# Kernel tuning notes

Measured on AMD Instinct MI355X. Metric: run time of the kernel, lower is better.

## Reference

```python
import jax, jax.numpy as jnp
import numpy as np

B, NQ, C, NH, NP = 4, 16384, 256, 8, 4
HH, WW = 128, 128
HD = C // NH


def setup_inputs() -> dict:
    key = jax.random.key(0)
    ks = jax.random.split(key, 10)
    s = 1.0 / np.sqrt(C)
    return {
        'query': jax.random.normal(ks[0], (B, NQ, C), jnp.float32),
        'reference_points': jax.random.uniform(ks[1], (B, NQ, 2), jnp.float32),
        'value': jax.random.normal(ks[2], (B, HH * WW, C), jnp.float32),
        'W_off': (jax.random.normal(ks[3], (C, NH * NP * 2), jnp.float32) * 0.01),
        'b_off': (jax.random.normal(ks[4], (NH * NP * 2,), jnp.float32) * 0.5),
        'W_attn': (jax.random.normal(ks[5], (C, NH * NP), jnp.float32) * s),
        'b_attn': jnp.zeros((NH * NP,), jnp.float32),
        'W_v': (jax.random.normal(ks[6], (C, C), jnp.float32) * s),
        'b_v': jnp.zeros((C,), jnp.float32),
        'W_out': (jax.random.normal(ks[7], (C, C), jnp.float32) * s),
        'b_out': jnp.zeros((C,), jnp.float32),
        'H': HH,
        'Wd': WW,
    }


def _deform_attn(query, reference_points, value, W_off, b_off, W_attn, b_attn,
                 W_v, b_v, W_out, b_out, H, W):
    Bb, Nq, Cc = query.shape
    dt = query.dtype
    # sampling offsets [B,Nq,NH,NP,2] and softmax attention weights [B,Nq,NH,NP]
    offsets = (query @ W_off + b_off).reshape(Bb, Nq, NH, NP, 2)
    attn = jax.nn.softmax((query @ W_attn + b_attn).reshape(Bb, Nq, NH, NP), axis=-1)
    offsets = offsets / jnp.array([W, H], dt) * jnp.asarray(0.1, dt)
    loc = jnp.clip(reference_points[:, :, None, None, :] + offsets, 0.0, 1.0)
    # value projection -> per-head spatial maps, flattened HW: [B,NH,H*W,HD]
    v = (value @ W_v + b_v).reshape(Bb, H, W, NH, HD)
    v = v.transpose(0, 3, 1, 2, 4).reshape(Bb, NH, H * W, HD)
    # grid_sample bilinear, align_corners=False, zero padding:
    # grid g = loc*2-1 ; pixel = ((g+1)*size - 1)/2 = loc*size - 0.5
    ix = loc[..., 0] * W - 0.5  # [B,Nq,NH,NP]
    iy = loc[..., 1] * H - 0.5
    x0 = jnp.floor(ix); y0 = jnp.floor(iy)
    wx = ix - x0; wy = iy - y0
    x0i = x0.astype(jnp.int32); y0i = y0.astype(jnp.int32)

    def corner(xc, yc, w):
        inb = ((xc >= 0) & (xc < W) & (yc >= 0) & (yc < H)).astype(dt)
        idx = jnp.clip(yc, 0, H - 1) * W + jnp.clip(xc, 0, W - 1)  # [B,Nq,NH,NP]
        idx = idx.transpose(0, 2, 1, 3).reshape(Bb, NH, Nq * NP)
        g = jnp.take_along_axis(v, idx[..., None], axis=2)  # [B,NH,Nq*NP,HD]
        g = g.reshape(Bb, NH, Nq, NP, HD)
        return g * (w * inb).transpose(0, 2, 1, 3)[..., None]

    one = jnp.asarray(1.0, dt)
    samp = (corner(x0i, y0i, (one - wx) * (one - wy))
            + corner(x0i + 1, y0i, wx * (one - wy))
            + corner(x0i, y0i + 1, (one - wx) * wy)
            + corner(x0i + 1, y0i + 1, wx * wy))  # [B,NH,Nq,NP,HD]
    # weighted sum over points, concat heads -> [B,Nq,C]
    out = jnp.einsum('bhnpd,bnhp->bnhd', samp, attn).reshape(Bb, Nq, Cc)
    return out @ W_out + b_out


def reference(query, reference_points, value, W_off, b_off, W_attn, b_attn,
              W_v, b_v, W_out, b_out, H, Wd):
    return _deform_attn(query, reference_points, value, W_off, b_off, W_attn,
                        b_attn, W_v, b_v, W_out, b_out, H, Wd)
```

## Files before the change

kernel.cpp:

```cpp
#include <hip/hip_runtime.h>
#include <hip/hip_bf16.h>

#define HWPIX  16384
#define MTOT   65536

typedef __attribute__((ext_vector_type(8))) __bf16 bf16x8;
typedef __attribute__((ext_vector_type(4))) __bf16 bf16x4;
typedef __attribute__((ext_vector_type(4))) float  f32x4;

#define GLOAD_LDS16(gsrc, ldst)                                                  \
    __builtin_amdgcn_global_load_lds(                                            \
        (const __attribute__((address_space(1))) void*)(gsrc),                   \
        (__attribute__((address_space(3))) void*)(ldst), 16, 0, 0)

__global__ void prep_weights(const float* __restrict__ Woff,
                             const float* __restrict__ Wattn,
                             const float* __restrict__ boff,
                             const float* __restrict__ battn,
                             const float* __restrict__ Wv,
                             const float* __restrict__ Wout,
                             __bf16* __restrict__ W1t,
                             __bf16* __restrict__ Wvt,
                             __bf16* __restrict__ Wot,
                             float* __restrict__ bias1)
{
    int tid = blockIdx.x * blockDim.x + threadIdx.x;
    int stride = gridDim.x * blockDim.x;
    for (int i = tid; i < 96 * 256; i += stride) {
        int n = i >> 8, k = i & 255;
        float v = (n < 64) ? Woff[k * 64 + n] : Wattn[k * 32 + (n - 64)];
        W1t[i] = (__bf16)v;
    }
    for (int i = tid; i < 256 * 256; i += stride) {
        int n = i >> 8, k = i & 255;
        Wvt[i] = (__bf16)Wv[k * 256 + n];
        Wot[i] = (__bf16)Wout[k * 256 + n];
    }
    for (int i = tid; i < 96; i += stride)
        bias1[i] = (i < 64) ? boff[i] : battn[i - 64];
}

__global__ __launch_bounds__(256, 4) void gemm96(
    const float* __restrict__ A,
    const __bf16* __restrict__ Bt,
    const float* __restrict__ bias,
    __bf16* __restrict__ P)
{
    constexpr int NF = 6;
    __shared__ __bf16 As[2][128 * 32];
    __shared__ __bf16 Bs[2][96 * 32];

    const int tid  = threadIdx.x;
    const int wave = tid >> 6, lane = tid & 63;
    const int r16  = lane & 15, kq = lane >> 4;
    const long mbase = (long)blockIdx.x * 128;

    const float* ap0 = A + (mbase + ((tid + 0 * 256) >> 3)) * 256 + (tid & 7) * 4;
    const float* ap1 = A + (mbase + ((tid + 1 * 256) >> 3)) * 256 + (tid & 7) * 4;
    const float* ap2 = A + (mbase + ((tid + 2 * 256) >> 3)) * 256 + (tid & 7) * 4;
    const float* ap3 = A + (mbase + ((tid + 3 * 256) >> 3)) * 256 + (tid & 7) * 4;
    const __bf16* bp0 = Bt + (long)(tid >> 2) * 256 + (tid & 3) * 8;
    const __bf16* bp1 = Bt + (long)((tid + 256) >> 2) * 256 + (tid & 3) * 8;

    f32x4 acc[2][NF];
#pragma unroll
    for (int m = 0; m < 2; ++m)
#pragma unroll
        for (int n = 0; n < NF; ++n) acc[m][n] = f32x4{0.f, 0.f, 0.f, 0.f};

    float4 ra0 = *(const float4*)ap0, ra1 = *(const float4*)ap1;
    float4 ra2 = *(const float4*)ap2, ra3 = *(const float4*)ap3;
    GLOAD_LDS16(bp0, &Bs[0][tid * 8]);
    if (tid < 128) GLOAD_LDS16(bp1, &Bs[0][(tid + 256) * 8]);
#define CW96(buf)                                                                 \
    {                                                                             \
        bf16x4 o;                                                                 \
        o[0] = (__bf16)ra0.x; o[1] = (__bf16)ra0.y; o[2] = (__bf16)ra0.z; o[3] = (__bf16)ra0.w; \
        *(bf16x4*)&As[buf][(tid + 0 * 256) * 4] = o;                              \
        o[0] = (__bf16)ra1.x; o[1] = (__bf16)ra1.y; o[2] = (__bf16)ra1.z; o[3] = (__bf16)ra1.w; \
        *(bf16x4*)&As[buf][(tid + 1 * 256) * 4] = o;                              \
        o[0] = (__bf16)ra2.x; o[1] = (__bf16)ra2.y; o[2] = (__bf16)ra2.z; o[3] = (__bf16)ra2.w; \
        *(bf16x4*)&As[buf][(tid + 2 * 256) * 4] = o;                              \
        o[0] = (__bf16)ra3.x; o[1] = (__bf16)ra3.y; o[2] = (__bf16)ra3.z; o[3] = (__bf16)ra3.w; \
        *(bf16x4*)&As[buf][(tid + 3 * 256) * 4] = o;                              \
    }
    CW96(0);
    __syncthreads();

    for (int t = 0; t < 8; ++t) {
        const int cur = t & 1, nxt = cur ^ 1;
        if (t < 7) {
            const int kt = (t + 1) * 32;
            ra0 = *(const float4*)(ap0 + kt);
            ra1 = *(const float4*)(ap1 + kt);
            ra2 = *(const float4*)(ap2 + kt);
            ra3 = *(const float4*)(ap3 + kt);
            GLOAD_LDS16(bp0 + kt, &Bs[nxt][tid * 8]);
            if (tid < 128) GLOAD_LDS16(bp1 + kt, &Bs[nxt][(tid + 256) * 8]);
        }
        bf16x8 aF0 = *(const bf16x8*)&As[cur][(wave * 32 + r16) * 32 + kq * 8];
        bf16x8 aF1 = *(const bf16x8*)&As[cur][(wave * 32 + 16 + r16) * 32 + kq * 8];
#pragma unroll
        for (int n = 0; n < NF; ++n) {
            bf16x8 bF = *(const bf16x8*)&Bs[cur][(n * 16 + r16) * 32 + kq * 8];
            acc[0][n] = __builtin_amdgcn_mfma_f32_16x16x32_bf16(aF0, bF, acc[0][n], 0, 0, 0);
            acc[1][n] = __builtin_amdgcn_mfma_f32_16x16x32_bf16(aF1, bF, acc[1][n], 0, 0, 0);
        }
        if (t < 7) CW96(nxt);
        __syncthreads();
    }

#pragma unroll
    for (int m = 0; m < 2; ++m) {
        long row0 = mbase + wave * 32 + m * 16 + kq * 4;
#pragma unroll
        for (int n = 0; n < NF; ++n) {
            int col = n * 16 + r16;
            float bz = bias[col];
#pragma unroll
            for (int r = 0; r < 4; ++r)
                P[(row0 + r) * 96 + col] = (__bf16)(acc[m][n][r] + bz);
        }
    }
}

__global__ __launch_bounds__(512, 4) void gemm256_v(
    const float* __restrict__ A,
    const __bf16* __restrict__ Bt,
    const float* __restrict__ bias,
    __bf16* __restrict__ Out)
{
    __shared__ __bf16 As[2][128 * 32];
    __shared__ __bf16 Bs[2][256 * 32];

    const int tid  = threadIdx.x;
    const int wave = tid >> 6, lane = tid & 63;
    const int r16  = lane & 15, kq = lane >> 4;
    const long mbase = (long)blockIdx.x * 128;

    const float* ap0 = A + (mbase + (tid >> 3)) * 256 + (tid & 7) * 4;
    const float* ap1 = ap0 + 64 * 256;
    const __bf16* bp0 = Bt + (long)(tid >> 2) * 256 + (tid & 3) * 8;
    const __bf16* bp1 = bp0 + 128 * 256;

    f32x4 acc[16];
#pragma unroll
    for (int n = 0; n < 16; ++n) acc[n] = f32x4{0.f, 0.f, 0.f, 0.f};

    float4 ra0 = *(const float4*)ap0, ra1 = *(const float4*)ap1;
    GLOAD_LDS16(bp0, &Bs[0][tid * 8]);
    GLOAD_LDS16(bp1, &Bs[0][(tid + 512) * 8]);
#define CW256(buf)                                                                \
    {                                                                             \
        bf16x4 o;                                                                 \
        o[0] = (__bf16)ra0.x; o[1] = (__bf16)ra0.y; o[2] = (__bf16)ra0.z; o[3] = (__bf16)ra0.w; \
        *(bf16x4*)&As[buf][tid * 4] = o;                                          \
        o[0] = (__bf16)ra1.x; o[1] = (__bf16)ra1.y; o[2] = (__bf16)ra1.z; o[3] = (__bf16)ra1.w; \
        *(bf16x4*)&As[buf][(tid + 512) * 4] = o;                                  \
    }
    CW256(0);
    __syncthreads();

    for (int t = 0; t < 8; ++t) {
        const int cur = t & 1, nxt = cur ^ 1;
        if (t < 7) {
            const int kt = (t + 1) * 32;
            ra0 = *(const float4*)(ap0 + kt);
            ra1 = *(const float4*)(ap1 + kt);
            GLOAD_LDS16(bp0 + kt, &Bs[nxt][tid * 8]);
            GLOAD_LDS16(bp1 + kt, &Bs[nxt][(tid + 512) * 8]);
        }
        bf16x8 aF = *(const bf16x8*)&As[cur][(wave * 16 + r16) * 32 + kq * 8];
#pragma unroll
        for (int n = 0; n < 16; ++n) {
            bf16x8 bF = *(const bf16x8*)&Bs[cur][(n * 16 + r16) * 32 + kq * 8];
            acc[n] = __builtin_amdgcn_mfma_f32_16x16x32_bf16(aF, bF, acc[n], 0, 0, 0);
        }
        if (t < 7) CW256(nxt);
        __syncthreads();
    }

    long row0 = mbase + wave * 16 + kq * 4;
#pragma unroll
    for (int n = 0; n < 16; ++n) {
        int col = n * 16 + r16;
        float bz = bias[col];
#pragma unroll
        for (int r = 0; r < 4; ++r)
            Out[(row0 + r) * 256 + col] = (__bf16)(acc[n][r] + bz);
    }
}

__global__ __launch_bounds__(512, 4) void sample_out_fused(
    const __bf16* __restrict__ P,
    const float* __restrict__ refp,
    const __bf16* __restrict__ vproj,
    const __bf16* __restrict__ Wot,
    const float* __restrict__ bias,
    float* __restrict__ Out)
{
    __shared__ __bf16 As[64 * 256];
    __shared__ __bf16 Bs[256 * 32];

    const int tid = threadIdx.x;
    const int bid = blockIdx.x;
    const int swz = (bid & 7) * 128 + (bid >> 3);
    const long qbase = (long)swz * 64;

    {
        const int g = tid >> 5, l = tid & 31;
        const int h = l >> 2, dg = l & 3;
        const char* vbase = (const char*)(vproj + ((qbase >> 14) << 14) * 256);
        const int chbyte = h * 64 + dg * 16;

        bf16x8 off8v[4];
        bf16x4 lg4v[4];
        float  rxv[4], ryv[4];
#pragma unroll
        for (int i = 0; i < 4; ++i) {
            const long q = qbase + g * 4 + i;
            off8v[i] = *(const bf16x8*)(P + q * 96 + h * 8);
            lg4v[i]  = *(const bf16x4*)(P + q * 96 + 64 + h * 4);
            rxv[i]   = refp[q * 2 + 0];
            ryv[i]   = refp[q * 2 + 1];
        }

#pragma unroll
        for (int i = 0; i < 4; ++i) {
            const int ql = g * 4 + i;
            bf16x8 off8 = off8v[i];
            float lg0 = (float)lg4v[i][0], lg1 = (float)lg4v[i][1];
            float lg2 = (float)lg4v[i][2], lg3 = (float)lg4v[i][3];
            const float rx = rxv[i], ry = ryv[i];
            float mx = fmaxf(fmaxf(lg0, lg1), fmaxf(lg2, lg3));
            float e0 = __expf(lg0 - mx), e1 = __expf(lg1 - mx);
            float e2 = __expf(lg2 - mx), e3 = __expf(lg3 - mx);
            float inv = 1.f / (e0 + e1 + e2 + e3);
            float at[4] = {e0 * inv, e1 * inv, e2 * inv, e3 * inv};

            float wxp[4], wyp[4];
            int x0p[4], y0p[4];
            int xmin = 127, ymin = 127;
#pragma unroll
            for (int p = 0; p < 4; ++p) {
                float ox = (float)off8[2 * p + 0] * (0.1f / 128.f);
                float oy = (float)off8[2 * p + 1] * (0.1f / 128.f);
                float lx = fminf(fmaxf(rx + ox, 0.f), 1.f);
                float ly = fminf(fmaxf(ry + oy, 0.f), 1.f);
                float ixf = lx * 128.f - 0.5f;
                float iyf = ly * 128.f - 0.5f;
                float xf = floorf(ixf), yf = floorf(iyf);
                wxp[p] = ixf - xf; wyp[p] = iyf - yf;
                x0p[p] = (int)xf;  y0p[p] = (int)yf;
                xmin = min(xmin, x0p[p]); ymin = min(ymin, y0p[p]);
            }
            float wc[3][3] = {{0.f,0.f,0.f},{0.f,0.f,0.f},{0.f,0.f,0.f}};
#pragma unroll
            for (int p = 0; p < 4; ++p) {
                int dx = min(x0p[p] - xmin, 1), dy = min(y0p[p] - ymin, 1);
                float wx = wxp[p], wy = wyp[p], ap = at[p];
                float xv0 = dx ? 0.f        : 1.f - wx;
                float xv1 = dx ? 1.f - wx   : wx;
                float xv2 = dx ? wx         : 0.f;
                float yv0 = (dy ? 0.f      : 1.f - wy) * ap;
                float yv1 = (dy ? 1.f - wy : wy)       * ap;
                float yv2 = (dy ? wy       : 0.f)      * ap;
                wc[0][0] += yv0 * xv0; wc[0][1] += yv0 * xv1; wc[0][2] += yv0 * xv2;
                wc[1][0] += yv1 * xv0; wc[1][1] += yv1 * xv1; wc[1][2] += yv1 * xv2;
                wc[2][0] += yv2 * xv0; wc[2][1] += yv2 * xv1; wc[2][2] += yv2 * xv2;
            }
            int   boff9[9];
            float w9[9];
#pragma unroll
            for (int r = 0; r < 3; ++r)
#pragma unroll
                for (int s = 0; s < 3; ++s) {
                    int py = ymin + r, px = xmin + s;
                    bool inb = (px >= 0) & (px < 128) & (py >= 0) & (py < 128);
                    int pyc = min(max(py, 0), 127), pxc = min(max(px, 0), 127);
                    boff9[r * 3 + s] = (pyc * 128 + pxc) * 512 + chbyte;
                    w9[r * 3 + s] = inb ? wc[r][s] : 0.f;
                }
            uint4 v[9];
#pragma unroll
            for (int j = 0; j < 9; ++j) v[j] = uint4{0u, 0u, 0u, 0u};
#pragma unroll
            for (int j = 0; j < 9; ++j)
                if (w9[j] != 0.f)
                    v[j] = *(const uint4*)(vbase + boff9[j]);

            float a[8];
#pragma unroll
            for (int j = 0; j < 8; ++j) a[j] = 0.f;
#pragma unroll
            for (int j = 0; j < 9; ++j) {
                float w = w9[j];
#pragma unroll
                for (int k = 0; k < 4; ++k) {
                    unsigned u = (&v[j].x)[k];
                    a[2 * k + 0] += w * __uint_as_float(u << 16);
                    a[2 * k + 1] += w * __uint_as_float(u & 0xFFFF0000u);
                }
            }
            bf16x8 o;
#pragma unroll
            for (int j = 0; j < 8; ++j) o[j] = (__bf16)a[j];
            int byte = ql * 512 + ((l * 16) ^ ((ql & 7) << 4));
            *(bf16x8*)((char*)As + byte) = o;
        }
    }

    const int wave = tid >> 6, lane = tid & 63;
    const int r16  = lane & 15, kq = lane >> 4;
    const int w4   = wave & 3, colh = wave >> 2;
    const int arow = w4 * 16 + r16;
    const int abase = arow * 512;
    const int aswz  = (arow & 7) << 4;

    f32x4 acc[8];
#pragma unroll
    for (int n = 0; n < 8; ++n) acc[n] = f32x4{0.f, 0.f, 0.f, 0.f};

    for (int kt = 0; kt < 256; kt += 32) {
        __syncthreads();
        for (int c = tid; c < 1024; c += 512)
            GLOAD_LDS16(Wot + (long)(c >> 2) * 256 + kt + (c & 3) * 8, &Bs[c * 8]);
        __syncthreads();
        bf16x8 aF = *(const bf16x8*)((char*)As + abase + ((kt * 2 + kq * 16) ^ aswz));
#pragma unroll
        for (int n = 0; n < 8; ++n) {
            bf16x8 bF = *(const bf16x8*)&Bs[(colh * 128 + n * 16 + r16) * 32 + kq * 8];
            acc[n] = __builtin_amdgcn_mfma_f32_16x16x32_bf16(aF, bF, acc[n], 0, 0, 0);
        }
    }

    long row0 = qbase + w4 * 16 + kq * 4;
#pragma unroll
    for (int n = 0; n < 8; ++n) {
        int col = colh * 128 + n * 16 + r16;
        float bz = bias[col];
#pragma unroll
        for (int r = 0; r < 4; ++r)
            Out[(row0 + r) * 256 + col] = acc[n][r] + bz;
    }
}

extern "C" void kernel_launch(void* const* d_in, const int* in_sizes, int n_in,
                              void* d_out, int out_size, void* d_ws, size_t ws_size,
                              hipStream_t stream)
{
    const float* query  = (const float*)d_in[0];
    const float* refp   = (const float*)d_in[1];
    const float* value  = (const float*)d_in[2];
    const float* W_off  = (const float*)d_in[3];
    const float* b_off  = (const float*)d_in[4];
    const float* W_attn = (const float*)d_in[5];
    const float* b_attn = (const float*)d_in[6];
    const float* W_v    = (const float*)d_in[7];
    const float* b_v    = (const float*)d_in[8];
    const float* W_out  = (const float*)d_in[9];
    const float* b_out  = (const float*)d_in[10];

    char* w = (char*)d_ws;
    __bf16* P       = (__bf16*)w;  w += (size_t)MTOT * 96 * 2;
    __bf16* vproj   = (__bf16*)w;  w += (size_t)MTOT * 256 * 2;
    __bf16* W1t     = (__bf16*)w;  w += 96 * 256 * 2;
    __bf16* Wvt     = (__bf16*)w;  w += 256 * 256 * 2;
    __bf16* Wot     = (__bf16*)w;  w += 256 * 256 * 2;
    float*  bias1   = (float*)w;   w += 96 * 4;

    prep_weights<<<120, 256, 0, stream>>>(W_off, W_attn, b_off, b_attn,
                                          W_v, W_out, W1t, Wvt, Wot, bias1);
    gemm96<<<MTOT / 128, 256, 0, stream>>>(query, W1t, bias1, P);
    gemm256_v<<<MTOT / 128, 512, 0, stream>>>(value, Wvt, b_v, vproj);
    sample_out_fused<<<MTOT / 64, 512, 0, stream>>>(P, refp, vproj, Wot, b_out,
                                                    (float*)d_out);
}
```

Baseline: 84.87 us.

## Read output-projection weights directly from global and raise occupancy in fused sampler

The fused sample+output-projection kernel no longer stages W_out tiles into LDS with per-k-tile barriers. Each MFMA B fragment is now loaded straight from global memory, relying on cache since W_out is small and shared by all blocks. The prefetch of per-query offsets and logits is un-batched to cut register pressure, and launch bounds ask for 8 blocks per CU instead of 4. This trades LDS reuse and coalesced staging for fewer barriers, less LDS use and higher occupancy, at the risk of more global/L2 traffic and less latency hiding in the gather loop.

```diff
diff --git a/kernel.cpp b/kernel.cpp
--- a/kernel.cpp
+++ b/kernel.cpp
@@ -191,7 +191,7 @@
     }
 }
 
-__global__ __launch_bounds__(512, 4) void sample_out_fused(
+__global__ __launch_bounds__(512, 8) void sample_out_fused(
     const __bf16* __restrict__ P,
     const float* __restrict__ refp,
     const __bf16* __restrict__ vproj,
@@ -200,7 +200,6 @@
     float* __restrict__ Out)
 {
     __shared__ __bf16 As[64 * 256];
-    __shared__ __bf16 Bs[256 * 32];
 
     const int tid = threadIdx.x;
     const int bid = blockIdx.x;
@@ -213,25 +212,16 @@
         const char* vbase = (const char*)(vproj + ((qbase >> 14) << 14) * 256);
         const int chbyte = h * 64 + dg * 16;
 
-        bf16x8 off8v[4];
-        bf16x4 lg4v[4];
-        float  rxv[4], ryv[4];
-#pragma unroll
         for (int i = 0; i < 4; ++i) {
-            const long q = qbase + g * 4 + i;
-            off8v[i] = *(const bf16x8*)(P + q * 96 + h * 8);
-            lg4v[i]  = *(const bf16x4*)(P + q * 96 + 64 + h * 4);
-            rxv[i]   = refp[q * 2 + 0];
-            ryv[i]   = refp[q * 2 + 1];
-        }
-
-#pragma unroll
-        for (int i = 0; i < 4; ++i) {
-            const int ql = g * 4 + i;
-            bf16x8 off8 = off8v[i];
-            float lg0 = (float)lg4v[i][0], lg1 = (float)lg4v[i][1];
-            float lg2 = (float)lg4v[i][2], lg3 = (float)lg4v[i][3];
-            const float rx = rxv[i], ry = ryv[i];
+            const int  ql = g * 4 + i;
+            const long q  = qbase + ql;
+            const __bf16* Pr = P + q * 96;
+            const float rx = refp[q * 2 + 0];
+            const float ry = refp[q * 2 + 1];
+            bf16x8 off8 = *(const bf16x8*)(Pr + h * 8);
+            bf16x4 lg4  = *(const bf16x4*)(Pr + 64 + h * 4);
+            float lg0 = (float)lg4[0], lg1 = (float)lg4[1];
+            float lg2 = (float)lg4[2], lg3 = (float)lg4[3];
             float mx = fmaxf(fmaxf(lg0, lg1), fmaxf(lg2, lg3));
             float e0 = __expf(lg0 - mx), e1 = __expf(lg1 - mx);
             float e2 = __expf(lg2 - mx), e3 = __expf(lg3 - mx);
@@ -289,26 +279,31 @@
                 if (w9[j] != 0.f)
                     v[j] = *(const uint4*)(vbase + boff9[j]);
 
-            float a[8];
-#pragma unroll
-            for (int j = 0; j < 8; ++j) a[j] = 0.f;
+            float2 a2[4];
+#pragma unroll
+            for (int k = 0; k < 4; ++k) a2[k] = float2{0.f, 0.f};
 #pragma unroll
             for (int j = 0; j < 9; ++j) {
                 float w = w9[j];
 #pragma unroll
                 for (int k = 0; k < 4; ++k) {
                     unsigned u = (&v[j].x)[k];
-                    a[2 * k + 0] += w * __uint_as_float(u << 16);
-                    a[2 * k + 1] += w * __uint_as_float(u & 0xFFFF0000u);
+                    a2[k].x += w * __uint_as_float(u << 16);
+                    a2[k].y += w * __uint_as_float(u & 0xFFFF0000u);
                 }
             }
             bf16x8 o;
 #pragma unroll
-            for (int j = 0; j < 8; ++j) o[j] = (__bf16)a[j];
+            for (int k = 0; k < 4; ++k) {
+                o[2 * k + 0] = (__bf16)a2[k].x;
+                o[2 * k + 1] = (__bf16)a2[k].y;
+            }
             int byte = ql * 512 + ((l * 16) ^ ((ql & 7) << 4));
             *(bf16x8*)((char*)As + byte) = o;
         }
     }
+
+    __syncthreads();
 
     const int wave = tid >> 6, lane = tid & 63;
     const int r16  = lane & 15, kq = lane >> 4;
@@ -322,14 +317,11 @@
     for (int n = 0; n < 8; ++n) acc[n] = f32x4{0.f, 0.f, 0.f, 0.f};
 
     for (int kt = 0; kt < 256; kt += 32) {
-        __syncthreads();
-        for (int c = tid; c < 1024; c += 512)
-            GLOAD_LDS16(Wot + (long)(c >> 2) * 256 + kt + (c & 3) * 8, &Bs[c * 8]);
-        __syncthreads();
         bf16x8 aF = *(const bf16x8*)((char*)As + abase + ((kt * 2 + kq * 16) ^ aswz));
 #pragma unroll
         for (int n = 0; n < 8; ++n) {
-            bf16x8 bF = *(const bf16x8*)&Bs[(colh * 128 + n * 16 + r16) * 32 + kq * 8];
+            bf16x8 bF = *(const bf16x8*)(Wot +
+                (long)(colh * 128 + n * 16 + r16) * 256 + kt + kq * 8);
             acc[n] = __builtin_amdgcn_mfma_f32_16x16x32_bf16(aF, bF, acc[n], 0, 0, 0);
         }
     }
```

After: 253.1 us. 2.98x slower.
